# Optimization experiments

Hardware: AMD Instinct MI355X
Metric: run time of the kernel (lower is better)

## Reference

```python
import jax, jax.numpy as jnp
import numpy as np

B, IMG, C = 128, 128, 3
NP = 8                      # n_patches per side
PS = IMG // NP              # patch size = 16
IN_D = C * PS * PS          # 768
E, NH, L, A = 768, 12, 12, 256
HS = E // NH                # 64
T = NP * NP + 1             # 65 tokens (cls + patches)
LN_EPS = 1e-5


def _pos_emb(seq_len, d):
    i = np.arange(seq_len, dtype=np.float64)[:, None]
    j = np.arange(d, dtype=np.float64)[None, :]
    even = np.sin(i / 10000 ** (j / d))
    odd = np.cos(i / 10000 ** ((j - 1) / d))
    return jnp.asarray(np.where(j % 2 == 0, even, odd), dtype=jnp.float32)


def setup_inputs() -> dict:
    key = jax.random.key(0)
    ks = jax.random.split(key, 16)
    s_e = 1.0 / np.sqrt(E)
    s_in = 1.0 / np.sqrt(IN_D)
    s_4e = 1.0 / np.sqrt(4 * E)
    return {
        "images": jax.random.normal(ks[0], (B, IMG, IMG, C), jnp.float32),
        "lin_w": jax.random.normal(ks[1], (IN_D, E), jnp.float32) * s_in,
        "cls_tok": jax.random.uniform(ks[2], (1, E), jnp.float32),
        "pos_emb": _pos_emb(T, E),
        "Wq": jax.random.normal(ks[3], (L, E, E), jnp.float32) * s_e,
        "Wk": jax.random.normal(ks[4], (L, E, E), jnp.float32) * s_e,
        "Wv": jax.random.normal(ks[5], (L, E, E), jnp.float32) * s_e,
        "Wo": jax.random.normal(ks[6], (L, E, E), jnp.float32) * s_e,
        "bo": jnp.zeros((L, E), jnp.float32),
        "ln1g": jnp.ones((L, E), jnp.float32),
        "ln1b": jnp.zeros((L, E), jnp.float32),
        "ln2g": jnp.ones((L, E), jnp.float32),
        "ln2b": jnp.zeros((L, E), jnp.float32),
        "W1": jax.random.normal(ks[7], (L, E, 4 * E), jnp.float32) * s_e,
        "b1": jnp.zeros((L, 4 * E), jnp.float32),
        "W2": jax.random.normal(ks[8], (L, 4 * E, E), jnp.float32) * s_4e,
        "b2": jnp.zeros((L, E), jnp.float32),
        "head_w": jax.random.normal(ks[9], (E, A), jnp.float32) * s_e,
        "head_b": jnp.zeros((A,), jnp.float32),
    }


def _layernorm(x, g, b):
    mu = jnp.mean(x, axis=-1, keepdims=True)
    var = jnp.var(x, axis=-1, keepdims=True)
    return (x - mu) * jax.lax.rsqrt(var + LN_EPS) * g + b


def _vit_forward(images, lin_w, cls_tok, pos_emb, Wq, Wk, Wv, Wo, bo,
                 ln1g, ln1b, ln2g, ln2b, W1, b1, W2, b2, head_w, head_b):
    n = images.shape[0]
    # patches: 'b (h p1) (w p2) c -> b (h w) (p1 p2 c)'
    p = images.reshape(n, NP, PS, NP, PS, C)
    patches = p.transpose(0, 1, 3, 2, 4, 5).reshape(n, NP * NP, IN_D)
    x = patches @ lin_w                                   # [B, 64, E]
    x = jnp.concatenate([jnp.broadcast_to(cls_tok, (n, 1, E)), x], axis=1)
    x = x + pos_emb[None]                                 # [B, T, E]

    scale = E ** (-0.5)  # NOTE: original scales by n_embd, not head_size

    def block(x, params):
        wq, wk, wv, wo_, bo_, g1, be1, g2, be2, w1, bb1, w2, bb2 = params
        h = _layernorm(x, g1, be1)
        q = (h @ wq).reshape(n, T, NH, HS)
        k = (h @ wk).reshape(n, T, NH, HS)
        v = (h @ wv).reshape(n, T, NH, HS)
        wei = jnp.einsum('bthd,bshd->bhts', q, k) * scale
        wei = jax.nn.softmax(wei, axis=-1)
        attn = jnp.einsum('bhts,bshd->bthd', wei, v).reshape(n, T, E)
        x = x + attn @ wo_ + bo_
        h2 = _layernorm(x, g2, be2)
        x = x + jax.nn.relu(h2 @ w1 + bb1) @ w2 + bb2
        return x, None

    x, _ = jax.lax.scan(block, x,
                        (Wq, Wk, Wv, Wo, bo, ln1g, ln1b, ln2g, ln2b,
                         W1, b1, W2, b2))
    cls = x[:, 0]                                          # [B, E]
    logits = jax.nn.softmax(cls @ head_w + head_b, axis=-1)  # model ends in Softmax
    return logits


def reference(images, lin_w, cls_tok, pos_emb, Wq, Wk, Wv, Wo, bo,
              ln1g, ln1b, ln2g, ln2b, W1, b1, W2, b2, head_w, head_b):
    return _vit_forward(images, lin_w, cls_tok, pos_emb, Wq, Wk, Wv, Wo, bo,
                        ln1g, ln1b, ln2g, ln2b, W1, b1, W2, b2, head_w, head_b)
```

## Files before the change

### kernel.cpp

```cpp
#include <hip/hip_runtime.h>
#include <cstdint>
#include <cstddef>


typedef __bf16 bf16x8 __attribute__((ext_vector_type(8)));
typedef float  f32x4  __attribute__((ext_vector_type(4)));

#define DEVINL __device__ __forceinline__

DEVINL uint16_t f2bf(float f){
  union U{float f; uint32_t i;} v; v.f=f; uint32_t u=v.i;
  return (uint16_t)((u + 0x7fffu + ((u>>16)&1u)) >> 16);
}

DEVINL void gl_lds16(const void* g, void* l){
  __builtin_amdgcn_global_load_lds((const __attribute__((address_space(1))) void*)g,
                                   (__attribute__((address_space(3))) void*)l, 16, 0, 0);
}

__global__ __launch_bounds__(256) void patchify_k(const float* __restrict__ img,
                                                  uint16_t* __restrict__ out){
  int i = blockIdx.x*256 + threadIdx.x;
  int m  = i / 768, kk = i - m*768;
  int b  = m >> 6,  t  = m & 63;
  int py = t >> 3,  px = t & 7;
  int r  = kk / 48, rem = kk - r*48;
  size_t src = ((size_t)(b*128 + py*16 + r)*128 + px*16)*3 + rem;
  out[i] = f2bf(img[src]);
}

DEVINL void tile_transpose(const float* __restrict__ src, uint16_t* __restrict__ dst,
                           int R, int C, int ti, int tj, int tid){
  __shared__ uint16_t tile[32][33];
  int tx = tid & 31, ty = tid >> 5;
  int r0 = ti*32, c0 = tj*32;
  #pragma unroll
  for (int i=0;i<4;++i)
    tile[ty+i*8][tx] = f2bf(src[(size_t)(r0+ty+i*8)*C + c0 + tx]);
  __syncthreads();
  #pragma unroll
  for (int i=0;i<4;++i)
    dst[(size_t)(c0+ty+i*8)*R + r0 + tx] = tile[tx][ty+i*8];
}

__global__ __launch_bounds__(256) void transpose_cvt_k(const float* __restrict__ src,
                                                       uint16_t* __restrict__ dst, int R, int C){
  tile_transpose(src, dst, R, C, blockIdx.y, blockIdx.x, threadIdx.x);
}

__global__ __launch_bounds__(256) void prep_layer_k(
    const float* __restrict__ Wq, const float* __restrict__ Wk,
    const float* __restrict__ Wv, const float* __restrict__ Wo,
    const float* __restrict__ W1, const float* __restrict__ W2,
    uint16_t* __restrict__ wbuf){
  int idx = blockIdx.x;
  const float* src; uint16_t* dst; int R, C, ti, tj;
  if (idx < 2304){
    int m = idx / 576, t = idx - m*576; ti = t/24; tj = t - ti*24; R=768; C=768;
    src = (m==0)?Wq:(m==1)?Wk:(m==2)?Wv:Wo;
    dst = wbuf + (size_t)m*589824;
  } else if (idx < 4608){
    int t = idx - 2304; ti = t/96; tj = t - ti*96; R=768; C=3072;
    src = W1; dst = wbuf + 2359296;
  } else {
    int t = idx - 4608; ti = t/24; tj = t - ti*24; R=3072; C=768;
    src = W2; dst = wbuf + 4718592;
  }
  tile_transpose(src, dst, R, C, ti, tj, threadIdx.x);
}

__global__ __launch_bounds__(256) void cls_init_k(const float* __restrict__ ct,
                                                  const float* __restrict__ pos,
                                                  float* __restrict__ X){
  int b = blockIdx.x, tid = threadIdx.x;
  for (int e = tid; e < 768; e += 256)
    X[(size_t)b*65*768 + e] = ct[e] + pos[e];
}

template<int SUMP>
__global__ __launch_bounds__(256) void ln_k(const float* __restrict__ Xin,
                                            float* __restrict__ Xout,
                                            const float* __restrict__ P1,
                                            uint16_t* __restrict__ H,
                                            const float* __restrict__ g,
                                            const float* __restrict__ b){
  int row = blockIdx.x, tid = threadIdx.x;
  const size_t ro = (size_t)row*768;
  const float* xr = Xin + ro;
  float v0, v1, v2;
  if constexpr (SUMP){
    const float* p1 = P1 + ro;
    v0 = xr[tid]     + p1[tid];
    v1 = xr[tid+256] + p1[tid+256];
    v2 = xr[tid+512] + p1[tid+512];
    float* xo = Xout + ro;
    xo[tid] = v0; xo[tid+256] = v1; xo[tid+512] = v2;
  } else {
    v0 = xr[tid]; v1 = xr[tid+256]; v2 = xr[tid+512];
  }
  int wid = tid>>6, lane = tid&63;
  __shared__ float part[4];
  __shared__ float bc[2];
  float s = v0+v1+v2;
  #pragma unroll
  for (int o=32;o;o>>=1) s += __shfl_down(s,o);
  if (lane==0) part[wid] = s;
  __syncthreads();
  if (tid==0) bc[0] = (part[0]+part[1]+part[2]+part[3]) * (1.f/768.f);
  __syncthreads();
  float mu = bc[0];
  float d0=v0-mu, d1=v1-mu, d2=v2-mu;
  float q = d0*d0 + d1*d1 + d2*d2;
  #pragma unroll
  for (int o=32;o;o>>=1) q += __shfl_down(q,o);
  __syncthreads();
  if (lane==0) part[wid] = q;
  __syncthreads();
  if (tid==0) bc[1] = rsqrtf((part[0]+part[1]+part[2]+part[3])*(1.f/768.f) + 1e-5f);
  __syncthreads();
  float rs = bc[1];
  uint16_t* hr = H + ro;
  hr[tid]     = f2bf(d0*rs*g[tid]     + b[tid]);
  hr[tid+256] = f2bf(d1*rs*g[tid+256] + b[tid+256]);
  hr[tid+512] = f2bf(d2*rs*g[tid+512] + b[tid+512]);
}

enum { EP_BF16=0, EP_RES=1, EP_RELU=2, EP_EMB=3 };

template<int MODE, int BN>
__global__ __launch_bounds__(256) void gemm_bt_k(
    const uint16_t* __restrict__ A, const uint16_t* __restrict__ Bt,
    int M, int N, int K, int strideB, long long strideO,
    const float* __restrict__ bias, float* __restrict__ X,
    uint16_t* __restrict__ Obf, const float* __restrict__ pos)
{
  constexpr int WN = BN/2;
  constexpr int NF = WN/16;
  constexpr int BLOADS = BN/64;
  __shared__ __align__(16) uint16_t sA[3][128*32];
  __shared__ __align__(16) uint16_t sB[3][BN*32];
  const int tid = threadIdx.x;
  const int wid = tid>>6, lane = tid&63;
  const int nx = gridDim.x;
  const int nwg = nx*gridDim.y;
  int idx = blockIdx.y*nx + blockIdx.x;
  int q8 = nwg>>3, r8 = nwg&7, xcd = idx&7, off = idx>>3;
  int swz = (xcd<r8 ? xcd*(q8+1) : r8*(q8+1) + (xcd-r8)*q8) + off;
  const int bn = (swz % nx)*BN, bm = (swz / nx)*128;
  const int z = blockIdx.z;
  const uint16_t* Bz = Bt + (size_t)z*strideB;
  const int wr = wid>>1, wc = wid&1;
  const int frow = lane&15, g = lane>>4;
  int srA[2], scA[2];
  #pragma unroll
  for (int rr=0; rr<2; ++rr){
    int G = rr*256 + tid;
    srA[rr] = G>>2; scA[rr] = ((G&3) - (G>>3)) & 3;
  }
  int srB[BLOADS], scB[BLOADS];
  #pragma unroll
  for (int rr=0; rr<BLOADS; ++rr){
    int G = rr*256 + tid;
    srB[rr] = G>>2; scB[rr] = ((G&3) - (G>>3)) & 3;
  }
  const int rsw = (frow>>1)&3;
  f32x4 acc[4][NF] = {};
  const int nt = K>>5;

  auto stage = [&](char* dA, char* dB, int k0){
    #pragma unroll
    for (int rr=0; rr<2; ++rr)
      gl_lds16(A + (size_t)(bm+srA[rr])*K + k0 + scA[rr]*8, dA + (rr*256 + wid*64)*16);
    #pragma unroll
    for (int rr=0; rr<BLOADS; ++rr)
      gl_lds16(Bz + (size_t)(bn+srB[rr])*K + k0 + scB[rr]*8, dB + (rr*256 + wid*64)*16);
  };

  char *cA=(char*)sA[0], *nA=(char*)sA[1], *fA=(char*)sA[2];
  char *cB=(char*)sB[0], *nB=(char*)sB[1], *fB=(char*)sB[2];
  stage(cA, cB, 0);
  stage(nA, nB, 32);

  for (int t = 0; t < nt; ++t){
    if (t+2 < nt){
      stage(fA, fB, (t+2)<<5);
      if constexpr (BLOADS==1) asm volatile("s_waitcnt vmcnt(6)" ::: "memory");
      else                     asm volatile("s_waitcnt vmcnt(8)" ::: "memory");
    } else if (t+1 < nt){
      if constexpr (BLOADS==1) asm volatile("s_waitcnt vmcnt(3)" ::: "memory");
      else                     asm volatile("s_waitcnt vmcnt(4)" ::: "memory");
    } else {
      asm volatile("s_waitcnt vmcnt(0)" ::: "memory");
    }
    __builtin_amdgcn_s_barrier();
    bf16x8 a[4], b[NF];
    #pragma unroll
    for (int m=0;m<4;++m)
      a[m] = *(const bf16x8*)(cA + (wr*64+m*16+frow)*64 + (((g+rsw)&3)<<4));
    #pragma unroll
    for (int n=0;n<NF;++n)
      b[n] = *(const bf16x8*)(cB + (wc*WN+n*16+frow)*64 + (((g+rsw)&3)<<4));
    #pragma unroll
    for (int m=0;m<4;++m)
      #pragma unroll
      for (int n=0;n<NF;++n)
        acc[m][n] = __builtin_amdgcn_mfma_f32_16x16x32_bf16(a[m], b[n], acc[m][n], 0,0,0);
    __builtin_amdgcn_s_barrier();
    char* t1=cA; cA=nA; nA=fA; fA=t1;
    char* t2=cB; cB=nB; nB=fB; fB=t2;
  }

  uint16_t* Oz = Obf + (size_t)z*(size_t)strideO;
  #pragma unroll
  for (int m=0;m<4;++m){
    int gr0 = bm + wr*64 + m*16 + (lane>>4)*4;
    #pragma unroll
    for (int n=0;n<NF;++n){
      int gc = bn + wc*WN + n*16 + (lane&15);
      #pragma unroll
      for (int r=0;r<4;++r){
        int grow = gr0 + r;
        float vsum = acc[m][n][r];
        if constexpr (MODE==EP_BF16){
          Oz[(size_t)grow*N + gc] = f2bf(vsum);
        } else if constexpr (MODE==EP_RES){
          X[(size_t)grow*N + gc] += vsum + bias[gc];
        } else if constexpr (MODE==EP_RELU){
          float u = vsum + bias[gc];
          Oz[(size_t)grow*N + gc] = f2bf(u > 0.f ? u : 0.f);
        } else {
          int t2i = grow & 63, bb = grow >> 6;
          X[((size_t)bb*65 + 1 + t2i)*768 + gc] = vsum + pos[(size_t)(t2i+1)*768 + gc];
        }
      }
    }
  }
}

template<int MODE, int SK>
__global__ __launch_bounds__(512) void gemm2m_k(
    const uint16_t* __restrict__ A, const uint16_t* __restrict__ Bt,
    int M, int N, int K, int strideB, long long strideO,
    const float* __restrict__ bias, float* __restrict__ X,
    uint16_t* __restrict__ Obf, float* __restrict__ P1)
{
  __shared__ __align__(16) uint16_t sA[2][256*32];
  __shared__ __align__(16) uint16_t sB[2][128*32];
  const int tid = threadIdx.x;
  const int wid = tid>>6, lane = tid&63;
  const int nx = gridDim.x;
  const int nwg = nx*gridDim.y;
  int idx = blockIdx.y*nx + blockIdx.x;
  int q8 = nwg>>3, r8 = nwg&7, xcd = idx&7, off = idx>>3;
  int swz = (xcd<r8 ? xcd*(q8+1) : r8*(q8+1) + (xcd-r8)*q8) + off;
  const int bn = (swz % nx)*128, bm = (swz / nx)*256;
  const int z = blockIdx.z;
  const uint16_t* Bz = (SK==1) ? Bt + (size_t)z*strideB : Bt;
  const int kbase = (SK==1) ? 0 : z*(K/SK);
  const int KS = (SK==1) ? K : K/SK;
  const int wr = wid>>1, wc = wid&1;
  const int frow = lane&15, g = lane>>4;
  int srA[2], scA[2];
  #pragma unroll
  for (int rr=0; rr<2; ++rr){
    int G = rr*512 + tid;
    srA[rr] = G>>2; scA[rr] = ((G&3) - (G>>3)) & 3;
  }
  const int srB = tid>>2, scB = ((tid&3) - (tid>>3)) & 3;
  const int rsw = (frow>>1)&3;
  f32x4 acc[4][4] = {};
  const int nt = KS>>5;

  auto stage = [&](int bsel, int k0){
    char* dA = (char*)sA[bsel]; char* dB = (char*)sB[bsel];
    #pragma unroll
    for (int rr=0; rr<2; ++rr)
      gl_lds16(A + (size_t)(bm+srA[rr])*K + kbase + k0 + scA[rr]*8,
               dA + (rr*512 + wid*64)*16);
    gl_lds16(Bz + (size_t)(bn+srB)*K + kbase + k0 + scB*8, dB + (wid*64)*16);
  };

  stage(0, 0);
  int buf = 0;
  for (int t = 0; t < nt; ++t){
    if (t+1 < nt){
      stage(buf^1, (t+1)<<5);
      asm volatile("s_waitcnt vmcnt(3)" ::: "memory");
    } else {
      asm volatile("s_waitcnt vmcnt(0)" ::: "memory");
    }
    __builtin_amdgcn_s_barrier();
    const char* sAc = (const char*)sA[buf];
    const char* sBc = (const char*)sB[buf];
    bf16x8 a[4], b[4];
    #pragma unroll
    for (int m=0;m<4;++m)
      a[m] = *(const bf16x8*)(sAc + (wr*64+m*16+frow)*64 + (((g+rsw)&3)<<4));
    #pragma unroll
    for (int n=0;n<4;++n)
      b[n] = *(const bf16x8*)(sBc + (wc*64+n*16+frow)*64 + (((g+rsw)&3)<<4));
    #pragma unroll
    for (int m=0;m<4;++m)
      #pragma unroll
      for (int n=0;n<4;++n)
        acc[m][n] = __builtin_amdgcn_mfma_f32_16x16x32_bf16(a[m], b[n], acc[m][n], 0,0,0);
    __builtin_amdgcn_s_barrier();
    buf ^= 1;
  }

  uint16_t* Oz = Obf + (size_t)z*(size_t)strideO;
  #pragma unroll
  for (int m=0;m<4;++m){
    int gr0 = bm + wr*64 + m*16 + (lane>>4)*4;
    #pragma unroll
    for (int n=0;n<4;++n){
      int gc = bn + wc*64 + n*16 + (lane&15);
      #pragma unroll
      for (int r=0;r<4;++r){
        int grow = gr0 + r;
        if (grow < M){
          float vsum = acc[m][n][r];
          if constexpr (MODE==EP_BF16){
            Oz[(size_t)grow*N + gc] = f2bf(vsum);
          } else if constexpr (MODE==EP_RES){
            if constexpr (SK==1){
              X[(size_t)grow*N + gc] += vsum + bias[gc];
            } else {
              if (z==0) X[(size_t)grow*N + gc] += vsum + bias[gc];
              else      P1[(size_t)grow*N + gc] = vsum;
            }
          } else if constexpr (MODE==EP_RELU){
            float u = vsum + bias[gc];
            Oz[(size_t)grow*N + gc] = f2bf(u > 0.f ? u : 0.f);
          }
        }
      }
    }
  }
}

__global__ __launch_bounds__(320) void attn_mfma_k(const uint16_t* __restrict__ q,
    const uint16_t* __restrict__ k, const uint16_t* __restrict__ v,
    uint16_t* __restrict__ o)
{
  __shared__ __align__(16) uint16_t P_lds[80][104];
  __shared__ __align__(16) uint16_t Vt[64][104];
  const int bh = blockIdx.x; const int b = bh / 12, hd = bh - b*12;
  const int tid = threadIdx.x;
  const int m = tid>>6;
  const int lane = tid&63;
  const int g = lane>>4, c = lane&15;
  const size_t base = (size_t)b*65*768 + (size_t)hd*64;

  for (int i = tid; i < 80*16; i += 320) P_lds[i>>4][80 + (i&15)] = 0;
  for (int i = tid; i < 64*32; i += 320) Vt[i>>5][64 + (i&31)] = 0;
  __syncthreads();
  for (int j = tid; j < 520; j += 320){
    int key = j >> 3, dc = j & 7;
    union { bf16x8 v8; uint16_t u[8]; } gv;
    gv.v8 = *(const bf16x8*)&v[base + (size_t)key*768 + dc*8];
    #pragma unroll
    for (int e = 0; e < 8; ++e) Vt[dc*8 + e][key] = gv.u[e];
  }

  bf16x8 bk[5][2];
  #pragma unroll
  for (int n=0;n<5;++n)
    #pragma unroll
    for (int kk=0;kk<2;++kk)
      bk[n][kk] = *(const bf16x8*)&k[base + (size_t)(n*16 + c)*768 + kk*32 + g*8];

  bf16x8 aq[2];
  #pragma unroll
  for (int kk=0;kk<2;++kk)
    aq[kk] = *(const bf16x8*)&q[base + (size_t)(m*16 + c)*768 + kk*32 + g*8];
  f32x4 sacc[5] = {};
  #pragma unroll
  for (int kk=0;kk<2;++kk)
    #pragma unroll
    for (int n=0;n<5;++n)
      sacc[n] = __builtin_amdgcn_mfma_f32_16x16x32_bf16(aq[kk], bk[n][kk], sacc[n], 0,0,0);

  const float scale = 0.03608439182435161f;
  #pragma unroll
  for (int r=0;r<4;++r){
    float val[5]; float mx = -3.0e38f;
    #pragma unroll
    for (int n=0;n<5;++n){
      val[n] = (n*16 + c) < 65 ? sacc[n][r]*scale : -3.0e38f;
      mx = fmaxf(mx, val[n]);
    }
    #pragma unroll
    for (int off=1; off<16; off<<=1) mx = fmaxf(mx, __shfl_xor(mx, off));
    float p[5], sum = 0.f;
    #pragma unroll
    for (int n=0;n<5;++n){
      p[n] = (n*16 + c) < 65 ? __expf(val[n]-mx) : 0.f;
      sum += p[n];
    }
    #pragma unroll
    for (int off=1; off<16; off<<=1) sum += __shfl_xor(sum, off);
    float rinv = 1.f / sum;
    int row = m*16 + g*4 + r;
    #pragma unroll
    for (int n=0;n<5;++n) P_lds[row][n*16 + c] = f2bf(p[n]*rinv);
  }
  __syncthreads();

  bf16x8 vb[4][3];
  #pragma unroll
  for (int n=0;n<4;++n)
    #pragma unroll
    for (int kk=0;kk<3;++kk)
      vb[n][kk] = *(const bf16x8*)&Vt[n*16 + c][kk*32 + g*8];
  f32x4 oacc[4] = {};
  #pragma unroll
  for (int kk=0;kk<3;++kk){
    bf16x8 pa = *(const bf16x8*)&P_lds[m*16 + c][kk*32 + g*8];
    #pragma unroll
    for (int n=0;n<4;++n)
      oacc[n] = __builtin_amdgcn_mfma_f32_16x16x32_bf16(pa, vb[n][kk], oacc[n], 0,0,0);
  }
  #pragma unroll
  for (int r=0;r<4;++r){
    int row = m*16 + g*4 + r;
    if (row < 65){
      #pragma unroll
      for (int n=0;n<4;++n)
        o[base + (size_t)row*768 + n*16 + c] = f2bf(oacc[n][r]);
    }
  }
}

__global__ __launch_bounds__(256) void head_k(const float* __restrict__ X,
    const float* __restrict__ P1,
    const float* __restrict__ W, const float* __restrict__ bias,
    float* __restrict__ out){
  int b = blockIdx.x, a = threadIdx.x;
  const size_t ro = (size_t)b*65*768;
  const float* xr = X + ro;
  const float* p1 = P1 + ro;
  float acc = bias[a];
  for (int kk=0; kk<768; ++kk)
    acc += (xr[kk]+p1[kk])*W[(size_t)kk*256 + a];
  int wid = a>>6, lane = a&63;
  __shared__ float red[4];
  float mx = acc;
  #pragma unroll
  for (int off=32; off; off>>=1) mx = fmaxf(mx, __shfl_xor(mx, off));
  if (lane==0) red[wid]=mx;
  __syncthreads();
  mx = fmaxf(fmaxf(red[0],red[1]), fmaxf(red[2],red[3]));
  float e = __expf(acc-mx);
  float s = e;
  #pragma unroll
  for (int off=32; off; off>>=1) s += __shfl_xor(s, off);
  __syncthreads();
  if (lane==0) red[wid]=s;
  __syncthreads();
  s = red[0]+red[1]+red[2]+red[3];
  out[(size_t)b*256 + a] = e/s;
}

extern "C" void kernel_launch(void* const* d_in, const int* in_sizes, int n_in,
                              void* d_out, int out_size, void* d_ws, size_t ws_size,
                              hipStream_t stream)
{
  const float* images = (const float*)d_in[0];
  const float* lin_w  = (const float*)d_in[1];
  const float* cls_tok= (const float*)d_in[2];
  const float* pos    = (const float*)d_in[3];
  const float* Wq = (const float*)d_in[4];
  const float* Wk = (const float*)d_in[5];
  const float* Wv = (const float*)d_in[6];
  const float* Wo = (const float*)d_in[7];
  const float* bo = (const float*)d_in[8];
  const float* ln1g=(const float*)d_in[9];
  const float* ln1b=(const float*)d_in[10];
  const float* ln2g=(const float*)d_in[11];
  const float* ln2b=(const float*)d_in[12];
  const float* W1 = (const float*)d_in[13];
  const float* b1 = (const float*)d_in[14];
  const float* W2 = (const float*)d_in[15];
  const float* b2 = (const float*)d_in[16];
  const float* hw = (const float*)d_in[17];
  const float* hb = (const float*)d_in[18];

  char* ws = (char*)d_ws;
  float*    x    = (float*)   (ws + 0);
  uint16_t* attn = (uint16_t*)(ws + 25559040);
  float*    P1   = (float*)   (ws + 25559040);
  uint16_t* qkv  = (uint16_t*)(ws + 38338560);
  uint16_t* h    = (uint16_t*)(ws + 76677120);
  uint16_t* mid  = (uint16_t*)(ws + 89456640);
  uint16_t* wbuf = (uint16_t*)(ws + 140574720);
  uint16_t* lwt  = (uint16_t*)(ws + 154730496);

  patchify_k<<<24576,256,0,stream>>>(images, mid);
  transpose_cvt_k<<<dim3(24,24),256,0,stream>>>(lin_w, lwt, 768, 768);
  gemm_bt_k<EP_EMB,64><<<dim3(12,64,1),256,0,stream>>>(mid, lwt, 8192,768,768, 0,0,
                                                   nullptr, x, nullptr, pos);
  cls_init_k<<<128,256,0,stream>>>(cls_tok, pos, x);

  for (int l=0;l<12;++l){
    prep_layer_k<<<6912,256,0,stream>>>(Wq+(size_t)l*589824, Wk+(size_t)l*589824,
                                        Wv+(size_t)l*589824, Wo+(size_t)l*589824,
                                        W1+(size_t)l*2359296, W2+(size_t)l*2359296, wbuf);
    if (l==0)
      ln_k<0><<<8320,256,0,stream>>>(x, nullptr, nullptr, h, ln1g, ln1b);
    else
      ln_k<1><<<8320,256,0,stream>>>(x, x, P1, h,
                                     ln1g+(size_t)l*768, ln1b+(size_t)l*768);
    gemm2m_k<EP_BF16,1><<<dim3(6,33,3),512,0,stream>>>(h, wbuf, 8320,768,768,
                                                       589824, 6389760LL,
                                                       nullptr, nullptr, qkv, nullptr);
    attn_mfma_k<<<1536,320,0,stream>>>(qkv, qkv+6389760, qkv+12779520, attn);
    gemm_bt_k<EP_RES,64><<<dim3(12,65,1),256,0,stream>>>(attn, wbuf+1769472, 8320,768,768,
                                                     0,0, bo+(size_t)l*768, x, nullptr, nullptr);
    ln_k<0><<<8320,256,0,stream>>>(x, nullptr, nullptr, h,
                                   ln2g+(size_t)l*768, ln2b+(size_t)l*768);
    gemm2m_k<EP_RELU,1><<<dim3(24,33,1),512,0,stream>>>(h, wbuf+2359296, 8320,3072,768,
                                                        0,0, b1+(size_t)l*3072, nullptr, mid, nullptr);
    gemm2m_k<EP_RES,2><<<dim3(6,33,2),512,0,stream>>>(mid, wbuf+4718592, 8320,768,3072,
                                                      0,0, b2+(size_t)l*768, x, nullptr, P1);
  }
  head_k<<<128,256,0,stream>>>(x, P1, hw, hb, (float*)d_out);
}
```

Baseline: 3.140 ms.

## Use 256x256 GEMM tiles with triple buffering and a fused QKV output

The 512-thread GEMM now uses 256x256 output tiles, with each wave computing 128x64, and a three-stage LDS pipeline so two loads stay in flight. It also raises MFMA wave priority with s_setprio. The QKV projection becomes a single N=2304 GEMM writing an interleaved [token, 2304] buffer, and attention indexes into it directly. The FFN2 split-K goes from 2 to 3, adding a P2 partial buffer that the next layernorm and the head fold in. The larger tiles cut redundant operand loads but give fewer workgroups and use more LDS and registers per block.

```diff
diff --git a/kernel.cpp b/kernel.cpp
--- a/kernel.cpp
+++ b/kernel.cpp
@@ -81,6 +81,7 @@
 __global__ __launch_bounds__(256) void ln_k(const float* __restrict__ Xin,
                                             float* __restrict__ Xout,
                                             const float* __restrict__ P1,
+                                            const float* __restrict__ P2,
                                             uint16_t* __restrict__ H,
                                             const float* __restrict__ g,
                                             const float* __restrict__ b){
@@ -89,10 +90,10 @@
   const float* xr = Xin + ro;
   float v0, v1, v2;
   if constexpr (SUMP){
-    const float* p1 = P1 + ro;
-    v0 = xr[tid]     + p1[tid];
-    v1 = xr[tid+256] + p1[tid+256];
-    v2 = xr[tid+512] + p1[tid+512];
+    const float* p1 = P1 + ro; const float* p2 = P2 + ro;
+    v0 = xr[tid]     + p1[tid]     + p2[tid];
+    v1 = xr[tid+256] + p1[tid+256] + p2[tid+256];
+    v2 = xr[tid+512] + p1[tid+512] + p2[tid+512];
     float* xo = Xout + ro;
     xo[tid] = v0; xo[tid+256] = v1; xo[tid+512] = v2;
   } else {
@@ -238,14 +239,14 @@
 }
 
 template<int MODE, int SK>
-__global__ __launch_bounds__(512) void gemm2m_k(
+__global__ __launch_bounds__(512) void gemm256_k(
     const uint16_t* __restrict__ A, const uint16_t* __restrict__ Bt,
-    int M, int N, int K, int strideB, long long strideO,
+    int M, int N, int K,
     const float* __restrict__ bias, float* __restrict__ X,
-    uint16_t* __restrict__ Obf, float* __restrict__ P1)
+    uint16_t* __restrict__ Obf, float* __restrict__ P1, float* __restrict__ P2)
 {
-  __shared__ __align__(16) uint16_t sA[2][256*32];
-  __shared__ __align__(16) uint16_t sB[2][128*32];
+  __shared__ __align__(16) uint16_t sA[3][256*32];
+  __shared__ __align__(16) uint16_t sB[3][256*32];
   const int tid = threadIdx.x;
   const int wid = tid>>6, lane = tid&63;
   const int nx = gridDim.x;
@@ -253,65 +254,69 @@
   int idx = blockIdx.y*nx + blockIdx.x;
   int q8 = nwg>>3, r8 = nwg&7, xcd = idx&7, off = idx>>3;
   int swz = (xcd<r8 ? xcd*(q8+1) : r8*(q8+1) + (xcd-r8)*q8) + off;
-  const int bn = (swz % nx)*128, bm = (swz / nx)*256;
+  const int bn = (swz % nx)*256, bm = (swz / nx)*256;
   const int z = blockIdx.z;
-  const uint16_t* Bz = (SK==1) ? Bt + (size_t)z*strideB : Bt;
   const int kbase = (SK==1) ? 0 : z*(K/SK);
   const int KS = (SK==1) ? K : K/SK;
-  const int wr = wid>>1, wc = wid&1;
+  const int wr = wid>>2, wc = wid&3;
   const int frow = lane&15, g = lane>>4;
-  int srA[2], scA[2];
+  int sr[2], sc[2];
   #pragma unroll
   for (int rr=0; rr<2; ++rr){
     int G = rr*512 + tid;
-    srA[rr] = G>>2; scA[rr] = ((G&3) - (G>>3)) & 3;
-  }
-  const int srB = tid>>2, scB = ((tid&3) - (tid>>3)) & 3;
+    sr[rr] = G>>2; sc[rr] = ((G&3) - (G>>3)) & 3;
+  }
   const int rsw = (frow>>1)&3;
-  f32x4 acc[4][4] = {};
+  f32x4 acc[8][4] = {};
   const int nt = KS>>5;
 
   auto stage = [&](int bsel, int k0){
     char* dA = (char*)sA[bsel]; char* dB = (char*)sB[bsel];
     #pragma unroll
-    for (int rr=0; rr<2; ++rr)
-      gl_lds16(A + (size_t)(bm+srA[rr])*K + kbase + k0 + scA[rr]*8,
+    for (int rr=0; rr<2; ++rr){
+      gl_lds16(A  + (size_t)(bm+sr[rr])*K + kbase + k0 + sc[rr]*8,
                dA + (rr*512 + wid*64)*16);
-    gl_lds16(Bz + (size_t)(bn+srB)*K + kbase + k0 + scB*8, dB + (wid*64)*16);
+      gl_lds16(Bt + (size_t)(bn+sr[rr])*K + kbase + k0 + sc[rr]*8,
+               dB + (rr*512 + wid*64)*16);
+    }
   };
 
   stage(0, 0);
-  int buf = 0;
+  stage(1, 32);
+  int cur = 0;
   for (int t = 0; t < nt; ++t){
-    if (t+1 < nt){
-      stage(buf^1, (t+1)<<5);
-      asm volatile("s_waitcnt vmcnt(3)" ::: "memory");
+    if (t+2 < nt){
+      stage((cur+2)%3, (t+2)<<5);
+      asm volatile("s_waitcnt vmcnt(8)" ::: "memory");
+    } else if (t+1 < nt){
+      asm volatile("s_waitcnt vmcnt(4)" ::: "memory");
     } else {
       asm volatile("s_waitcnt vmcnt(0)" ::: "memory");
     }
     __builtin_amdgcn_s_barrier();
-    const char* sAc = (const char*)sA[buf];
-    const char* sBc = (const char*)sB[buf];
-    bf16x8 a[4], b[4];
-    #pragma unroll
-    for (int m=0;m<4;++m)
-      a[m] = *(const bf16x8*)(sAc + (wr*64+m*16+frow)*64 + (((g+rsw)&3)<<4));
+    const char* sAc = (const char*)sA[cur];
+    const char* sBc = (const char*)sB[cur];
+    bf16x8 a[8], b[4];
+    #pragma unroll
+    for (int m=0;m<8;++m)
+      a[m] = *(const bf16x8*)(sAc + (wr*128+m*16+frow)*64 + (((g+rsw)&3)<<4));
     #pragma unroll
     for (int n=0;n<4;++n)
       b[n] = *(const bf16x8*)(sBc + (wc*64+n*16+frow)*64 + (((g+rsw)&3)<<4));
-    #pragma unroll
-    for (int m=0;m<4;++m)
+    __builtin_amdgcn_s_setprio(1);
+    #pragma unroll
+    for (int m=0;m<8;++m)
       #pragma unroll
       for (int n=0;n<4;++n)
         acc[m][n] = __builtin_amdgcn_mfma_f32_16x16x32_bf16(a[m], b[n], acc[m][n], 0,0,0);
+    __builtin_amdgcn_s_setprio(0);
     __builtin_amdgcn_s_barrier();
-    buf ^= 1;
-  }
-
-  uint16_t* Oz = Obf + (size_t)z*(size_t)strideO;
-  #pragma unroll
-  for (int m=0;m<4;++m){
-    int gr0 = bm + wr*64 + m*16 + (lane>>4)*4;
+    cur = (cur+1)%3;
+  }
+
+  #pragma unroll
+  for (int m=0;m<8;++m){
+    int gr0 = bm + wr*128 + m*16 + (lane>>4)*4;
     #pragma unroll
     for (int n=0;n<4;++n){
       int gc = bn + wc*64 + n*16 + (lane&15);
@@ -321,17 +326,14 @@
         if (grow < M){
           float vsum = acc[m][n][r];
           if constexpr (MODE==EP_BF16){
-            Oz[(size_t)grow*N + gc] = f2bf(vsum);
+            Obf[(size_t)grow*N + gc] = f2bf(vsum);
           } else if constexpr (MODE==EP_RES){
-            if constexpr (SK==1){
-              X[(size_t)grow*N + gc] += vsum + bias[gc];
-            } else {
-              if (z==0) X[(size_t)grow*N + gc] += vsum + bias[gc];
-              else      P1[(size_t)grow*N + gc] = vsum;
-            }
+            if (z==0)      X[(size_t)grow*N + gc] += vsum + bias[gc];
+            else if (z==1) P1[(size_t)grow*N + gc] = vsum;
+            else           P2[(size_t)grow*N + gc] = vsum;
           } else if constexpr (MODE==EP_RELU){
             float u = vsum + bias[gc];
-            Oz[(size_t)grow*N + gc] = f2bf(u > 0.f ? u : 0.f);
+            Obf[(size_t)grow*N + gc] = f2bf(u > 0.f ? u : 0.f);
           }
         }
       }
@@ -339,8 +341,7 @@
   }
 }
 
-__global__ __launch_bounds__(320) void attn_mfma_k(const uint16_t* __restrict__ q,
-    const uint16_t* __restrict__ k, const uint16_t* __restrict__ v,
+__global__ __launch_bounds__(320) void attn_mfma_k(const uint16_t* __restrict__ qkv,
     uint16_t* __restrict__ o)
 {
   __shared__ __align__(16) uint16_t P_lds[80][104];
@@ -350,7 +351,8 @@
   const int m = tid>>6;
   const int lane = tid&63;
   const int g = lane>>4, c = lane&15;
-  const size_t base = (size_t)b*65*768 + (size_t)hd*64;
+  const size_t base  = (size_t)b*65*2304 + (size_t)hd*64;
+  const size_t obase = (size_t)b*65*768  + (size_t)hd*64;
 
   for (int i = tid; i < 80*16; i += 320) P_lds[i>>4][80 + (i&15)] = 0;
   for (int i = tid; i < 64*32; i += 320) Vt[i>>5][64 + (i&31)] = 0;
@@ -358,7 +360,7 @@
   for (int j = tid; j < 520; j += 320){
     int key = j >> 3, dc = j & 7;
     union { bf16x8 v8; uint16_t u[8]; } gv;
-    gv.v8 = *(const bf16x8*)&v[base + (size_t)key*768 + dc*8];
+    gv.v8 = *(const bf16x8*)&qkv[base + 1536 + (size_t)key*2304 + dc*8];
     #pragma unroll
     for (int e = 0; e < 8; ++e) Vt[dc*8 + e][key] = gv.u[e];
   }
@@ -368,12 +370,12 @@
   for (int n=0;n<5;++n)
     #pragma unroll
     for (int kk=0;kk<2;++kk)
-      bk[n][kk] = *(const bf16x8*)&k[base + (size_t)(n*16 + c)*768 + kk*32 + g*8];
+      bk[n][kk] = *(const bf16x8*)&qkv[base + 768 + (size_t)(n*16 + c)*2304 + kk*32 + g*8];
 
   bf16x8 aq[2];
   #pragma unroll
   for (int kk=0;kk<2;++kk)
-    aq[kk] = *(const bf16x8*)&q[base + (size_t)(m*16 + c)*768 + kk*32 + g*8];
+    aq[kk] = *(const bf16x8*)&qkv[base + (size_t)(m*16 + c)*2304 + kk*32 + g*8];
   f32x4 sacc[5] = {};
   #pragma unroll
   for (int kk=0;kk<2;++kk)
@@ -427,22 +429,23 @@
     if (row < 65){
       #pragma unroll
       for (int n=0;n<4;++n)
-        o[base + (size_t)row*768 + n*16 + c] = f2bf(oacc[n][r]);
+        o[obase + (size_t)row*768 + n*16 + c] = f2bf(oacc[r==r?r:r, oacc[n][r]*0.f==0.f ? n : n][r]);
     }
   }
 }
 
 __global__ __launch_bounds__(256) void head_k(const float* __restrict__ X,
-    const float* __restrict__ P1,
+    const float* __restrict__ P1, const float* __restrict__ P2,
     const float* __restrict__ W, const float* __restrict__ bias,
     float* __restrict__ out){
   int b = blockIdx.x, a = threadIdx.x;
   const size_t ro = (size_t)b*65*768;
   const float* xr = X + ro;
   const float* p1 = P1 + ro;
+  const float* p2 = P2 + ro;
   float acc = bias[a];
   for (int kk=0; kk<768; ++kk)
-    acc += (xr[kk]+p1[kk])*W[(size_t)kk*256 + a];
+    acc += (xr[kk]+p1[kk]+p2[kk])*W[(size_t)kk*256 + a];
   int wid = a>>6, lane = a&63;
   __shared__ float red[4];
   float mx = acc;
@@ -491,6 +494,7 @@
   uint16_t* attn = (uint16_t*)(ws + 25559040);
   float*    P1   = (float*)   (ws + 25559040);
   uint16_t* qkv  = (uint16_t*)(ws + 38338560);
+  float*    P2   = (float*)   (ws + 51118080);
   uint16_t* h    = (uint16_t*)(ws + 76677120);
   uint16_t* mid  = (uint16_t*)(ws + 89456640);
   uint16_t* wbuf = (uint16_t*)(ws + 140574720);
@@ -507,22 +511,21 @@
                                         Wv+(size_t)l*589824, Wo+(size_t)l*589824,
                                         W1+(size_t)l*2359296, W2+(size_t)l*2359296, wbuf);
     if (l==0)
-      ln_k<0><<<8320,256,0,stream>>>(x, nullptr, nullptr, h, ln1g, ln1b);
+      ln_k<0><<<8320,256,0,stream>>>(x, nullptr, nullptr, nullptr, h, ln1g, ln1b);
     else
-      ln_k<1><<<8320,256,0,stream>>>(x, x, P1, h,
+      ln_k<1><<<8320,256,0,stream>>>(x, x, P1, P2, h,
                                      ln1g+(size_t)l*768, ln1b+(size_t)l*768);
-    gemm2m_k<EP_BF16,1><<<dim3(6,33,3),512,0,stream>>>(h, wbuf, 8320,768,768,
-                                                       589824, 6389760LL,
-                                                       nullptr, nullptr, qkv, nullptr);
-    attn_mfma_k<<<1536,320,0,stream>>>(qkv, qkv+6389760, qkv+12779520, attn);
+    gemm256_k<EP_BF16,1><<<dim3(9,33,1),512,0,stream>>>(h, wbuf, 8320,2304,768,
+                                                        nullptr, nullptr, qkv, nullptr, nullptr);
+    attn_mfma_k<<<1536,320,0,stream>>>(qkv, attn);
     gemm_bt_k<EP_RES,64><<<dim3(12,65,1),256,0,stream>>>(attn, wbuf+1769472, 8320,768,768,
                                                      0,0, bo+(size_t)l*768, x, nullptr, nullptr);
-    ln_k<0><<<8320,256,0,stream>>>(x, nullptr, nullptr, h,
+    ln_k<0><<<8320,256,0,stream>>>(x, nullptr, nullptr, nullptr, h,
                                    ln2g+(size_t)l*768, ln2b+(size_t)l*768);
-    gemm2m_k<EP_RELU,1><<<dim3(24,33,1),512,0,stream>>>(h, wbuf+2359296, 8320,3072,768,
-                                                        0,0, b1+(size_t)l*3072, nullptr, mid, nullptr);
-    gemm2m_k<EP_RES,2><<<dim3(6,33,2),512,0,stream>>>(mid, wbuf+4718592, 8320,768,3072,
-                                                      0,0, b2+(size_t)l*768, x, nullptr, P1);
-  }
-  head_k<<<128,256,0,stream>>>(x, P1, hw, hb, (float*)d_out);
-}
+    gemm256_k<EP_RELU,1><<<dim3(12,33,1),512,0,stream>>>(h, wbuf+2359296, 8320,3072,768,
+                                                         b1+(size_t)l*3072, nullptr, mid, nullptr, nullptr);
+    gemm256_k<EP_RES,3><<<dim3(3,33,3),512,0,stream>>>(mid, wbuf+4718592, 8320,768,3072,
+                                                       b2+(size_t)l*768, x, nullptr, P1, P2);
+  }
+  head_k<<<128,256,0,stream>>>(x, P1, P2, hw, hb, (float*)d_out);
+}
```

Result: slower. 4.448 ms (+41.7%).
